# Performance work log

Hardware: AMD Instinct MI355X
Metric: run time of the kernel (lower is better)

Reference implementation:

```python
import jax, jax.numpy as jnp
import numpy as np

IMG, P, C = 224, 16, 3
D, H, MLP = 512, 8, 2048
L, NCLS = 10, 10      # budget, classes
N = (IMG // P) ** 2   # 196 patches
PD = C * P * P        # patch_dim = 768


def setup_inputs() -> dict:
    key = jax.random.key(0)
    ks = jax.random.split(key, 32)
    w = lambda k, shape: (jax.random.normal(k, shape, jnp.float32) * 0.02)
    return {
        'x': jax.random.normal(ks[0], (32, C, IMG, IMG), jnp.float32),
        'y': jax.random.randint(ks[1], (32, 1), 0, NCLS),
        'pos_emb': w(ks[2], (1, N + 1, D)),
        'cls_tok': w(ks[3], (1, 1, D)),
        'Wp': w(ks[4], (D, PD)), 'bp': jnp.zeros((D,), jnp.float32),
        'Wqkv': w(ks[5], (3 * D, D)),
        'Wo': w(ks[6], (D, D)), 'bo': jnp.zeros((D,), jnp.float32),
        'ln1_g': jnp.ones((D,), jnp.float32), 'ln1_b': jnp.zeros((D,), jnp.float32),
        'ln2_g': jnp.ones((D,), jnp.float32), 'ln2_b': jnp.zeros((D,), jnp.float32),
        'W1': w(ks[7], (MLP, D)), 'b1': jnp.zeros((MLP,), jnp.float32),
        'W2': w(ks[8], (D, MLP)), 'b2': jnp.zeros((D,), jnp.float32),
        'lnh_g': jnp.ones((D,), jnp.float32), 'lnh_b': jnp.zeros((D,), jnp.float32),
        'Wh1': w(ks[9], (MLP, D)), 'bh1': jnp.zeros((MLP,), jnp.float32),
        'Wh2': w(ks[10], (1, MLP)), 'bh2': jnp.zeros((1,), jnp.float32),
        'lnc_g': jnp.ones((D,), jnp.float32), 'lnc_b': jnp.zeros((D,), jnp.float32),
        'Wc1': w(ks[11], (MLP, D)), 'bc1': jnp.zeros((MLP,), jnp.float32),
        'Wc2': w(ks[12], (NCLS, MLP)), 'bc2': jnp.zeros((NCLS,), jnp.float32),
    }


def _ln(u, g, b):
    mu = u.mean(-1, keepdims=True)
    v = ((u - mu) ** 2).mean(-1, keepdims=True)
    return (u - mu) / jnp.sqrt(v + 1e-5) * g + b


def _gelu(u):
    return jax.nn.gelu(u, approximate=False)


def reference(x, y, pos_emb, cls_tok, Wp, bp, Wqkv, Wo, bo,
              ln1_g, ln1_b, ln2_g, ln2_b, W1, b1, W2, b2,
              lnh_g, lnh_b, Wh1, bh1, Wh2, bh2,
              lnc_g, lnc_b, Wc1, bc1, Wc2, bc2):
    b = x.shape[0]
    hp = IMG // P
    # patchify: b c (h p1) (w p2) -> b (h w) (p1 p2 c)
    xp = x.reshape(b, C, hp, P, hp, P).transpose(0, 2, 4, 3, 5, 1).reshape(b, N, PD)
    e = xp @ Wp.T + bp                                   # [b, N, D]
    z = jnp.concatenate([jnp.broadcast_to(cls_tok, (b, 1, D)), e], 1) + pos_emb[:, :N + 1]

    scale = D ** -0.5

    def attn(u):
        q, k, v = jnp.split(u @ Wqkv.T, 3, axis=-1)
        hsplit = lambda t: t.reshape(b, -1, H, D // H).transpose(0, 2, 1, 3)  # b h n d
        q, k, v = hsplit(q), hsplit(k), hsplit(v)
        a = jax.nn.softmax(jnp.einsum('bhid,bhjd->bhij', q, k) * scale, axis=-1)
        o = jnp.einsum('bhij,bhjd->bhid', a, v).transpose(0, 2, 1, 3).reshape(b, -1, D)
        return o @ Wo.T + bo

    def ff(u):
        return _gelu(u @ W1.T + b1) @ W2.T + b2

    def halt(u):
        h = _gelu(_ln(u, lnh_g, lnh_b) @ Wh1.T + bh1) @ Wh2.T + bh2  # [b, n, 1]
        return jax.nn.sigmoid(h).mean(1)[:, 0]                        # [b]

    def step(u, _):
        u = u + attn(_ln(u, ln1_g, ln1_b))
        u = u + ff(_ln(u, ln2_g, ln2_b))
        return u, (u[:, 0], halt(u))

    _, (cls_outs, halts) = jax.lax.scan(step, z, None, length=L)
    cls_outs = cls_outs.transpose(1, 0, 2)   # [b, L, D]
    halts = halts.T                          # [b, L]

    logits = _gelu(_ln(cls_outs, lnc_g, lnc_b) @ Wc1.T + bc1) @ Wc2.T + bc2  # [b, L, 10]
    logp = jax.nn.log_softmax(logits, -1)
    lab = y[:, 0]
    ce = -jnp.take_along_axis(logp, jnp.broadcast_to(lab[:, None, None], (b, L, 1)), axis=2)[..., 0]  # [b, L]

    idx = jnp.argmin(ce, axis=1) + 1                     # [b], halting step per sample
    steps = jnp.arange(L)
    mask = (steps[None, :] < idx[:, None]).astype(ce.dtype)
    denom = idx.astype(ce.dtype)
    ref_ce = (ce * mask).sum(1) / denom                  # per-sample mean over first idx steps

    # halt labels: 1 for steps < idx-1, 0 at step idx-1 (only first idx entries count)
    hl = jnp.where(steps[None, :] == (idx[:, None] - 1), 0.0, 1.0)
    p = jnp.clip(halts, 1e-7, 1.0 - 1e-7)
    bce = -(hl * jnp.log(p) + (1.0 - hl) * jnp.log1p(-p))
    halt_loss = (bce * mask).sum(1) / denom

    return ref_ce.mean() + halt_loss.mean()
```

## Files before the change

kernel.cpp:

```cpp
#include <hip/hip_runtime.h>
#include <math.h>

#define BBATCH 32
#define NTOK 197
#define NPATCH 196
#define PDIM 768
#define DDIM 512
#define NHEAD 8
#define DHEAD 64
#define MLPDIM 2048
#define NLAYER 10
#define NCLASS 10
#define MTOK (BBATCH*NTOK)
#define MPAD 6400
#define MPATCH (BBATCH*NPATCH)
#define QKVROWS (MTOK + 16)

typedef unsigned short u16;
typedef __attribute__((ext_vector_type(8))) short bf16x8;
typedef __attribute__((ext_vector_type(4))) float f32x4;
typedef __attribute__((ext_vector_type(8))) unsigned short ushort8;

__device__ __forceinline__ float gelu_f(float x) {
    return 0.5f * x * (1.0f + erff(x * 0.70710678118654752440f));
}
__device__ __forceinline__ float bf2f(u16 u) {
    union { unsigned int i; float f; } v; v.i = ((unsigned int)u) << 16; return v.f;
}
__device__ __forceinline__ u16 f2bf(float f) {
    union { float f; unsigned int u; } v; v.f = f;
    unsigned int r = v.u + 0x7FFFu + ((v.u >> 16) & 1u);
    return (u16)(r >> 16);
}
__device__ __forceinline__ void gload_lds16(const u16* g, u16* l) {
    __builtin_amdgcn_global_load_lds((const __attribute__((address_space(1))) void*)g,
                                     (__attribute__((address_space(3))) void*)l, 16, 0, 0);
}

template<int ACT, int HASB, int HASR, int OUTBF>
__global__ __launch_bounds__(256)
void mgemm_kernel(const u16* __restrict__ A, const u16* __restrict__ W,
                  const float* __restrict__ bias, const float* __restrict__ res,
                  void* __restrict__ Cout, int M, int Nn, int K)
{
    __shared__ u16 As[128 * 64];
    __shared__ u16 Bs[128 * 64];
    const int tid = threadIdx.x;
    const int lane = tid & 63;
    const int wid = tid >> 6;
    const int wr = wid >> 1, wc = wid & 1;
    const int m0 = blockIdx.y * 128, n0 = blockIdx.x * 128;

    f32x4 acc[4][4] = {};

    const int srow = tid >> 3;
    const int dcb  = (tid & 7) << 4;

    for (int k0 = 0; k0 < K; k0 += 64) {
        __syncthreads();
        #pragma unroll
        for (int p = 0; p < 4; ++p) {
            int r = p * 32 + srow;
            int scb = dcb ^ ((r & 7) << 4);
            gload_lds16(A + (size_t)(m0 + r) * K + k0 + (scb >> 1), &As[p * 2048 + tid * 8]);
            gload_lds16(W + (size_t)(n0 + r) * K + k0 + (scb >> 1), &Bs[p * 2048 + tid * 8]);
        }
        __syncthreads();

        #pragma unroll
        for (int kk = 0; kk < 64; kk += 32) {
            const int kb = (kk + ((lane >> 4) << 3)) << 1;
            bf16x8 af[4], bfr[4];
            #pragma unroll
            for (int mi = 0; mi < 4; ++mi) {
                int ar = wr * 64 + mi * 16 + (lane & 15);
                af[mi] = *(const bf16x8*)&As[ar * 64 + ((kb ^ ((ar & 7) << 4)) >> 1)];
            }
            #pragma unroll
            for (int ni = 0; ni < 4; ++ni) {
                int br = wc * 64 + ni * 16 + (lane & 15);
                bfr[ni] = *(const bf16x8*)&Bs[br * 64 + ((kb ^ ((br & 7) << 4)) >> 1)];
            }
            #pragma unroll
            for (int mi = 0; mi < 4; ++mi)
                #pragma unroll
                for (int ni = 0; ni < 4; ++ni)
                    acc[mi][ni] = __builtin_amdgcn_mfma_f32_16x16x32_bf16(
                        af[mi], bfr[ni], acc[mi][ni], 0, 0, 0);
        }
    }

    float* outf = (float*)Cout;
    u16*   outb = (u16*)Cout;
    #pragma unroll
    for (int mi = 0; mi < 4; ++mi) {
        #pragma unroll
        for (int j = 0; j < 4; ++j) {
            int row = m0 + wr * 64 + mi * 16 + ((lane >> 4) << 2) + j;
            if (row >= M) continue;
            #pragma unroll
            for (int ni = 0; ni < 4; ++ni) {
                int col = n0 + wc * 64 + ni * 16 + (lane & 15);
                float v = acc[mi][ni][j];
                if (HASB) v += bias[col];
                if (ACT)  v = gelu_f(v);
                if (HASR) v += res[(size_t)row * Nn + col];
                if (OUTBF) outb[(size_t)row * Nn + col] = f2bf(v);
                else       outf[(size_t)row * Nn + col] = v;
            }
        }
    }
}

__global__ __launch_bounds__(256)
void f2bf_kernel(const float* __restrict__ in, u16* __restrict__ out, int n4)
{
    int i = blockIdx.x * 256 + threadIdx.x;
    if (i >= n4) return;
    float4 v = ((const float4*)in)[i];
    u16 o0 = f2bf(v.x), o1 = f2bf(v.y), o2 = f2bf(v.z), o3 = f2bf(v.w);
    out[i * 4 + 0] = o0; out[i * 4 + 1] = o1; out[i * 4 + 2] = o2; out[i * 4 + 3] = o3;
}

__global__ __launch_bounds__(256)
void ln_kernel(const float* __restrict__ X, const float* __restrict__ g,
               const float* __restrict__ bb, u16* __restrict__ Y, int M)
{
    int wave = (blockIdx.x * 4) + (threadIdx.x >> 6);
    int lane = threadIdx.x & 63;
    if (wave >= M) return;
    const float* x = X + (size_t)wave * DDIM;
    float v[8];
    float s = 0.0f;
    #pragma unroll
    for (int i = 0; i < 8; i++) { v[i] = x[lane + i * 64]; s += v[i]; }
    #pragma unroll
    for (int off = 32; off; off >>= 1) s += __shfl_xor(s, off, 64);
    float mu = s * (1.0f / 512.0f);
    float q = 0.0f;
    #pragma unroll
    for (int i = 0; i < 8; i++) { float d = v[i] - mu; q += d * d; }
    #pragma unroll
    for (int off = 32; off; off >>= 1) q += __shfl_xor(q, off, 64);
    float inv = 1.0f / sqrtf(q * (1.0f / 512.0f) + 1e-5f);
    u16* y = Y + (size_t)wave * DDIM;
    #pragma unroll
    for (int i = 0; i < 8; i++) {
        int c = lane + i * 64;
        y[c] = f2bf((v[i] - mu) * inv * g[c] + bb[c]);
    }
}

__global__ __launch_bounds__(256)
void patch_kernel(const float* __restrict__ x, u16* __restrict__ xp)
{
    size_t idx = (size_t)blockIdx.x * 256 + threadIdx.x;
    if (idx >= (size_t)MPATCH * PDIM) return;
    int pd = (int)(idx % PDIM);
    int bn = (int)(idx / PDIM);
    int n = bn % NPATCH, b = bn / NPATCH;
    int c = pd % 3, pix = pd / 3;
    int px = pix % 16, py = pix / 16;
    int hx = n % 14, hy = n / 14;
    int row = hy * 16 + py, col = hx * 16 + px;
    xp[idx] = f2bf(x[((size_t)(b * 3 + c) * 224 + row) * 224 + col]);
}

__global__ __launch_bounds__(256)
void assemble_kernel(const float* __restrict__ e, const float* __restrict__ clstok,
                     const float* __restrict__ pos, float* __restrict__ U)
{
    size_t idx = (size_t)blockIdx.x * 256 + threadIdx.x;
    if (idx >= (size_t)MTOK * DDIM) return;
    int d = (int)(idx % DDIM);
    int bt = (int)(idx / DDIM);
    int t = bt % NTOK, b = bt / NTOK;
    float v = (t == 0) ? clstok[d] : e[((size_t)b * NPATCH + (t - 1)) * DDIM + d];
    U[idx] = v + pos[t * DDIM + d];
}

__global__ __launch_bounds__(256)
void attn_mfma_kernel(const u16* __restrict__ qkv, u16* __restrict__ O)
{
    __shared__ u16 Ks[208 * 64];
    __shared__ u16 Vt[64 * 208];
    __shared__ u16 Pl[4 * 16 * 208];

    const int bh = blockIdx.x >> 1;
    const int half = blockIdx.x & 1;
    const int b = bh >> 3, h = bh & 7;
    const int tid = threadIdx.x;
    const int lane = tid & 63, wid = tid >> 6;
    const size_t base = ((size_t)b * NTOK) * 1536 + (size_t)h * 64;

    {
        int j0 = tid >> 3;
        int d0 = (tid & 7) * 8;
        for (int p = 0; p < 7; ++p) {
            int j = p * 32 + j0;
            if (j < 208) {
                bf16x8 v = {};
                if (j < NTOK) v = *(const bf16x8*)&qkv[base + (size_t)j * 1536 + 512 + d0];
                int byt = (j * 128 + d0 * 2) ^ ((j & 7) << 4);
                *(bf16x8*)((char*)Ks + byt) = v;
            }
        }
    }
    {
        int d = tid & 63;
        int jg = tid >> 6;
        for (int j = jg * 52; j < jg * 52 + 52; ++j) {
            u16 v = (j < NTOK) ? qkv[base + (size_t)j * 1536 + 1024 + d] : (u16)0;
            int byt = (d * 416 + j * 2) ^ ((d & 7) << 4);
            *(u16*)((char*)Vt + byt) = v;
        }
    }
    __syncthreads();

    u16* Pw = Pl + wid * 16 * 208;
    const float scale = 0.04419417382415922f;
    const int t0   = half ? 7 : 0;
    const int tcnt = half ? 6 : 7;
    const int g = lane >> 4;
    const int mycol = lane & 15;

    for (int ti = wid; ti < tcnt; ti += 4) {
        const int r0 = (t0 + ti) * 16;
        bf16x8 qf[2];
        #pragma unroll
        for (int ks = 0; ks < 2; ++ks) {
            int row = r0 + mycol;
            int col = ks * 32 + (g << 3);
            qf[ks] = *(const bf16x8*)&qkv[base + (size_t)row * 1536 + col];
        }
        f32x4 s[13];
        #pragma unroll
        for (int ct = 0; ct < 13; ++ct) s[ct] = (f32x4){0.f, 0.f, 0.f, 0.f};
        #pragma unroll
        for (int ks = 0; ks < 2; ++ks) {
            int kbyte = (ks * 32 + (g << 3)) * 2;
            #pragma unroll
            for (int ct = 0; ct < 13; ++ct) {
                int n = ct * 16 + mycol;
                bf16x8 kf = *(const bf16x8*)((char*)Ks + ((n * 128 + kbyte) ^ ((n & 7) << 4)));
                s[ct] = __builtin_amdgcn_mfma_f32_16x16x32_bf16(qf[ks], kf, s[ct], 0, 0, 0);
            }
        }
        float m[4], sum[4];
        #pragma unroll
        for (int j = 0; j < 4; ++j) m[j] = -1e30f;
        #pragma unroll
        for (int ct = 0; ct < 13; ++ct) {
            bool valid = (ct * 16 + mycol) < NTOK;
            #pragma unroll
            for (int j = 0; j < 4; ++j) {
                float v = valid ? s[ct][j] * scale : -1e30f;
                s[ct][j] = v;
                m[j] = fmaxf(m[j], v);
            }
        }
        #pragma unroll
        for (int off = 1; off < 16; off <<= 1)
            #pragma unroll
            for (int j = 0; j < 4; ++j) m[j] = fmaxf(m[j], __shfl_xor(m[j], off, 64));
        #pragma unroll
        for (int j = 0; j < 4; ++j) sum[j] = 0.0f;
        #pragma unroll
        for (int ct = 0; ct < 13; ++ct)
            #pragma unroll
            for (int j = 0; j < 4; ++j) {
                float e = expf(s[ct][j] - m[j]);
                s[ct][j] = e;
                sum[j] += e;
            }
        #pragma unroll
        for (int off = 1; off < 16; off <<= 1)
            #pragma unroll
            for (int j = 0; j < 4; ++j) sum[j] += __shfl_xor(sum[j], off, 64);
        float inv[4];
        #pragma unroll
        for (int j = 0; j < 4; ++j) inv[j] = 1.0f / sum[j];
        #pragma unroll
        for (int ct = 0; ct < 13; ++ct) {
            int col = ct * 16 + mycol;
            #pragma unroll
            for (int j = 0; j < 4; ++j) {
                int row = (g << 2) + j;
                int byt = (row * 416 + col * 2) ^ ((row & 7) << 4);
                *(u16*)((char*)Pw + byt) = f2bf(s[ct][j] * inv[j]);
            }
        }
        #pragma unroll
        for (int nt = 0; nt < 4; ++nt) {
            f32x4 o = (f32x4){0.f, 0.f, 0.f, 0.f};
            #pragma unroll
            for (int ks = 0; ks < 7; ++ks) {
                bf16x8 pf = {}, vf = {};
                bool live = !(ks == 6 && g >= 2);
                if (live) {
                    int kbyte = (ks * 32 + (g << 3)) * 2;
                    pf = *(const bf16x8*)((char*)Pw + ((mycol * 416 + kbyte) ^ ((mycol & 7) << 4)));
                    int vrow = nt * 16 + mycol;
                    vf = *(const bf16x8*)((char*)Vt + ((vrow * 416 + kbyte) ^ ((vrow & 7) << 4)));
                }
                o = __builtin_amdgcn_mfma_f32_16x16x32_bf16(pf, vf, o, 0, 0, 0);
            }
            #pragma unroll
            for (int j = 0; j < 4; ++j) {
                int grow = r0 + (g << 2) + j;
                if (grow < NTOK)
                    O[((size_t)b * NTOK + grow) * DDIM + h * 64 + nt * 16 + mycol] = f2bf(o[j]);
            }
        }
    }
}

__global__ __launch_bounds__(256)
void halt_dot_kernel(const u16* __restrict__ Hh, const float* __restrict__ Wh2,
                     const float* __restrict__ bh2, float* __restrict__ hsc)
{
    int wave = (blockIdx.x * 4) + (threadIdx.x >> 6);
    int lane = threadIdx.x & 63;
    if (wave >= MTOK) return;
    const u16* row = Hh + (size_t)wave * MLPDIM;
    float s = 0.0f;
    #pragma unroll
    for (int i = 0; i < 4; i++) {
        ushort8 v = *(const ushort8*)&row[i * 512 + lane * 8];
        #pragma unroll
        for (int j = 0; j < 8; j++)
            s = fmaf(bf2f(v[j]), Wh2[i * 512 + lane * 8 + j], s);
    }
    #pragma unroll
    for (int off = 32; off; off >>= 1) s += __shfl_xor(s, off, 64);
    if (lane == 0) hsc[wave] = 1.0f / (1.0f + expf(-(s + bh2[0])));
}

__global__ __launch_bounds__(64)
void halt_mean_cls_kernel(const float* __restrict__ hsc, const float* __restrict__ U,
                          float* __restrict__ halts, float* __restrict__ cls, int l)
{
    int b = blockIdx.x, lane = threadIdx.x;
    float s = 0.0f;
    for (int t = lane; t < NTOK; t += 64) s += hsc[b * NTOK + t];
    #pragma unroll
    for (int off = 32; off; off >>= 1) s += __shfl_xor(s, off, 64);
    if (lane == 0) halts[b * NLAYER + l] = s * (1.0f / (float)NTOK);
    for (int d = lane; d < DDIM; d += 64)
        cls[((size_t)b * NLAYER + l) * DDIM + d] = U[(size_t)b * NTOK * DDIM + d];
}

__global__ __launch_bounds__(256)
void head_logits_kernel(const u16* __restrict__ Hh, const float* __restrict__ Wc2,
                        const float* __restrict__ bc2, float* __restrict__ logits)
{
    int wave = (blockIdx.x * 4) + (threadIdx.x >> 6);
    int lane = threadIdx.x & 63;
    if (wave >= BBATCH * NLAYER) return;
    const u16* row = Hh + (size_t)wave * MLPDIM;
    float rv[32];
    #pragma unroll
    for (int i = 0; i < 32; i++) rv[i] = bf2f(row[lane + i * 64]);
    #pragma unroll
    for (int c = 0; c < NCLASS; c++) {
        float s = 0.0f;
        #pragma unroll
        for (int i = 0; i < 32; i++) s = fmaf(rv[i], Wc2[c * MLPDIM + lane + i * 64], s);
        #pragma unroll
        for (int off = 32; off; off >>= 1) s += __shfl_xor(s, off, 64);
        if (lane == 0) logits[wave * NCLASS + c] = s + bc2[c];
    }
}

__global__ __launch_bounds__(256)
void ce_kernel(const float* __restrict__ logits, const int* __restrict__ y,
               float* __restrict__ ce)
{
    int r = blockIdx.x * 256 + threadIdx.x;
    if (r >= BBATCH * NLAYER) return;
    const float* lg = logits + (size_t)r * NCLASS;
    float mx = lg[0];
    #pragma unroll
    for (int i = 1; i < NCLASS; i++) mx = fmaxf(mx, lg[i]);
    float s = 0.0f;
    #pragma unroll
    for (int i = 0; i < NCLASS; i++) s += expf(lg[i] - mx);
    int lab = y[r / NLAYER];
    ce[r] = -(lg[lab] - mx - logf(s));
}

__global__ __launch_bounds__(64)
void loss_kernel(const float* __restrict__ ce, const float* __restrict__ halts,
                 float* __restrict__ out)
{
    int b = threadIdx.x;
    float total = 0.0f;
    if (b < BBATCH) {
        const float* c = ce + b * NLAYER;
        int idx = 0; float mn = c[0];
        for (int l = 1; l < NLAYER; l++) if (c[l] < mn) { mn = c[l]; idx = l; }
        idx += 1;
        float acc = 0.0f;
        for (int l = 0; l < idx; l++) {
            acc += c[l];
            float p = halts[b * NLAYER + l];
            p = fminf(fmaxf(p, 1e-7f), 1.0f - 1e-7f);
            float hl = (l == idx - 1) ? 0.0f : 1.0f;
            acc += -(hl * logf(p) + (1.0f - hl) * log1pf(-p));
        }
        total = acc / (float)idx;
    }
    #pragma unroll
    for (int off = 32; off; off >>= 1) total += __shfl_xor(total, off, 64);
    if (threadIdx.x == 0) out[0] = total * (1.0f / (float)BBATCH);
}

extern "C" void kernel_launch(void* const* d_in, const int* in_sizes, int n_in,
                              void* d_out, int out_size, void* d_ws, size_t ws_size,
                              hipStream_t stream)
{
    const float* x      = (const float*)d_in[0];
    const int*   y      = (const int*)d_in[1];
    const float* pos    = (const float*)d_in[2];
    const float* clstok = (const float*)d_in[3];
    const float* Wp     = (const float*)d_in[4];
    const float* bp     = (const float*)d_in[5];
    const float* Wqkv   = (const float*)d_in[6];
    const float* Wo     = (const float*)d_in[7];
    const float* bo     = (const float*)d_in[8];
    const float* ln1g   = (const float*)d_in[9];
    const float* ln1b   = (const float*)d_in[10];
    const float* ln2g   = (const float*)d_in[11];
    const float* ln2b   = (const float*)d_in[12];
    const float* W1     = (const float*)d_in[13];
    const float* b1     = (const float*)d_in[14];
    const float* W2     = (const float*)d_in[15];
    const float* b2     = (const float*)d_in[16];
    const float* lnhg   = (const float*)d_in[17];
    const float* lnhb   = (const float*)d_in[18];
    const float* Wh1    = (const float*)d_in[19];
    const float* bh1    = (const float*)d_in[20];
    const float* Wh2    = (const float*)d_in[21];
    const float* bh2    = (const float*)d_in[22];
    const float* lncg   = (const float*)d_in[23];
    const float* lncb   = (const float*)d_in[24];
    const float* Wc1    = (const float*)d_in[25];
    const float* bc1    = (const float*)d_in[26];
    const float* Wc2    = (const float*)d_in[27];
    const float* bc2    = (const float*)d_in[28];

    float* U      = (float*)d_ws;
    float* EMB    = U + (size_t)MTOK * DDIM;
    float* CLS    = EMB + (size_t)MPATCH * DDIM;
    float* LOGITS = CLS + (size_t)BBATCH * NLAYER * DDIM;
    float* CE     = LOGITS + BBATCH * NLAYER * NCLASS;
    float* HSC    = CE + BBATCH * NLAYER;
    float* HALTS  = HSC + MTOK;
    u16* QKVb = (u16*)(HALTS + BBATCH * NLAYER + 32);
    u16* LNB  = QKVb + (size_t)QKVROWS * 1536;
    u16* HB   = LNB + (size_t)MPAD * DDIM;
    u16* XP   = HB + (size_t)MPAD * MLPDIM;
    u16* CLNB = XP + (size_t)MPATCH * PDIM;
    u16* wWp  = CLNB + 384 * DDIM;
    u16* wWqkv= wWp   + 512 * 768;
    u16* wWo  = wWqkv + 1536 * 512;
    u16* wW1  = wWo   + 512 * 512;
    u16* wW2  = wW1   + 2048 * 512;
    u16* wWh1 = wW2   + 512 * 2048;
    u16* wWc1 = wWh1  + 2048 * 512;

    dim3 blk(256);

    f2bf_kernel<<<dim3((512*768/4 + 255)/256), blk, 0, stream>>>(Wp, wWp, 512*768/4);
    f2bf_kernel<<<dim3((1536*512/4 + 255)/256), blk, 0, stream>>>(Wqkv, wWqkv, 1536*512/4);
    f2bf_kernel<<<dim3((512*512/4 + 255)/256), blk, 0, stream>>>(Wo, wWo, 512*512/4);
    f2bf_kernel<<<dim3((2048*512/4 + 255)/256), blk, 0, stream>>>(W1, wW1, 2048*512/4);
    f2bf_kernel<<<dim3((512*2048/4 + 255)/256), blk, 0, stream>>>(W2, wW2, 512*2048/4);
    f2bf_kernel<<<dim3((2048*512/4 + 255)/256), blk, 0, stream>>>(Wh1, wWh1, 2048*512/4);
    f2bf_kernel<<<dim3((2048*512/4 + 255)/256), blk, 0, stream>>>(Wc1, wWc1, 2048*512/4);

    patch_kernel<<<dim3(((size_t)MPATCH * PDIM + 255) / 256), blk, 0, stream>>>(x, XP);
    mgemm_kernel<0,1,0,0><<<dim3(DDIM/128, MPATCH/128), blk, 0, stream>>>(
        XP, wWp, bp, nullptr, (void*)EMB, MPATCH, DDIM, PDIM);
    assemble_kernel<<<dim3(((size_t)MTOK * DDIM + 255) / 256), blk, 0, stream>>>(
        EMB, clstok, pos, U);

    const int MT = (MTOK + 127) / 128;

    for (int l = 0; l < NLAYER; l++) {
        ln_kernel<<<dim3((MTOK + 3) / 4), blk, 0, stream>>>(U, ln1g, ln1b, LNB, MTOK);
        mgemm_kernel<0,0,0,1><<<dim3(1536/128, MT), blk, 0, stream>>>(
            LNB, wWqkv, nullptr, nullptr, (void*)QKVb, MTOK, 1536, DDIM);
        attn_mfma_kernel<<<dim3(512), blk, 0, stream>>>(QKVb, LNB);
        mgemm_kernel<0,1,1,0><<<dim3(DDIM/128, MT), blk, 0, stream>>>(
            LNB, wWo, bo, U, (void*)U, MTOK, DDIM, DDIM);
        ln_kernel<<<dim3((MTOK + 3) / 4), blk, 0, stream>>>(U, ln2g, ln2b, LNB, MTOK);
        mgemm_kernel<1,1,0,1><<<dim3(MLPDIM/128, MT), blk, 0, stream>>>(
            LNB, wW1, b1, nullptr, (void*)HB, MTOK, MLPDIM, DDIM);
        mgemm_kernel<0,1,1,0><<<dim3(DDIM/128, MT), blk, 0, stream>>>(
            HB, wW2, b2, U, (void*)U, MTOK, DDIM, MLPDIM);
        ln_kernel<<<dim3((MTOK + 3) / 4), blk, 0, stream>>>(U, lnhg, lnhb, LNB, MTOK);
        mgemm_kernel<1,1,0,1><<<dim3(MLPDIM/128, MT), blk, 0, stream>>>(
            LNB, wWh1, bh1, nullptr, (void*)HB, MTOK, MLPDIM, DDIM);
        halt_dot_kernel<<<dim3((MTOK + 3) / 4), blk, 0, stream>>>(HB, Wh2, bh2, HSC);
        halt_mean_cls_kernel<<<dim3(BBATCH), dim3(64), 0, stream>>>(HSC, U, HALTS, CLS, l);
    }

    ln_kernel<<<dim3((BBATCH * NLAYER + 3) / 4), blk, 0, stream>>>(
        CLS, lncg, lncb, CLNB, BBATCH * NLAYER);
    mgemm_kernel<1,1,0,1><<<dim3(MLPDIM/128, 3), blk, 0, stream>>>(
        CLNB, wWc1, bc1, nullptr, (void*)HB, BBATCH * NLAYER, MLPDIM, DDIM);
    head_logits_kernel<<<dim3((BBATCH * NLAYER + 3) / 4), blk, 0, stream>>>(
        HB, Wc2, bc2, LOGITS);
    ce_kernel<<<dim3(2), blk, 0, stream>>>(LOGITS, y, CE);
    loss_kernel<<<dim3(1), dim3(64), 0, stream>>>(CE, HALTS, (float*)d_out);
}
```

Before: 2.419 ms.

## Double-buffer GEMM LDS tiles and fuse halt dot-product into halt GEMM epilogue

The GEMM kernel now uses two LDS buffers, so the next K-tile is loaded while the current one is computed, with a single barrier per iteration. The halting head's second linear layer is folded into the Wh1 GEMM epilogue. Each block computes gelu(acc+bias)·Wh2 partial sums, reduces them across lanes and atomically adds them into a per-token score zeroed by a memset. The sigmoid then moves into the halt-mean kernel. This removes the bf16 HB write and re-read plus a kernel launch, but doubles LDS use (lower occupancy risk) and adds float atomics, which make the summation order non-deterministic.

After: 2.342 ms. 3.2% less time.

```diff
diff --git a/kernel.cpp b/kernel.cpp
--- a/kernel.cpp
+++ b/kernel.cpp
@@ -37,14 +37,14 @@
                                      (__attribute__((address_space(3))) void*)l, 16, 0, 0);
 }
 
-template<int ACT, int HASB, int HASR, int OUTBF>
+template<int ACT, int HASB, int HASR, int OUTBF, int HALT>
 __global__ __launch_bounds__(256)
 void mgemm_kernel(const u16* __restrict__ A, const u16* __restrict__ W,
                   const float* __restrict__ bias, const float* __restrict__ res,
                   void* __restrict__ Cout, int M, int Nn, int K)
 {
-    __shared__ u16 As[128 * 64];
-    __shared__ u16 Bs[128 * 64];
+    __shared__ u16 As[2][128 * 64];
+    __shared__ u16 Bs[2][128 * 64];
     const int tid = threadIdx.x;
     const int lane = tid & 63;
     const int wid = tid >> 6;
@@ -56,17 +56,16 @@
     const int srow = tid >> 3;
     const int dcb  = (tid & 7) << 4;
 
-    for (int k0 = 0; k0 < K; k0 += 64) {
-        __syncthreads();
+    auto stage = [&](int buf, int k0) {
         #pragma unroll
         for (int p = 0; p < 4; ++p) {
             int r = p * 32 + srow;
             int scb = dcb ^ ((r & 7) << 4);
-            gload_lds16(A + (size_t)(m0 + r) * K + k0 + (scb >> 1), &As[p * 2048 + tid * 8]);
-            gload_lds16(W + (size_t)(n0 + r) * K + k0 + (scb >> 1), &Bs[p * 2048 + tid * 8]);
-        }
-        __syncthreads();
-
+            gload_lds16(A + (size_t)(m0 + r) * K + k0 + (scb >> 1), &As[buf][p * 2048 + tid * 8]);
+            gload_lds16(W + (size_t)(n0 + r) * K + k0 + (scb >> 1), &Bs[buf][p * 2048 + tid * 8]);
+        }
+    };
+    auto compute = [&](int buf) {
         #pragma unroll
         for (int kk = 0; kk < 64; kk += 32) {
             const int kb = (kk + ((lane >> 4) << 3)) << 1;
@@ -74,12 +73,12 @@
             #pragma unroll
             for (int mi = 0; mi < 4; ++mi) {
                 int ar = wr * 64 + mi * 16 + (lane & 15);
-                af[mi] = *(const bf16x8*)&As[ar * 64 + ((kb ^ ((ar & 7) << 4)) >> 1)];
+                af[mi] = *(const bf16x8*)&As[buf][ar * 64 + ((kb ^ ((ar & 7) << 4)) >> 1)];
             }
             #pragma unroll
             for (int ni = 0; ni < 4; ++ni) {
                 int br = wc * 64 + ni * 16 + (lane & 15);
-                bfr[ni] = *(const bf16x8*)&Bs[br * 64 + ((kb ^ ((br & 7) << 4)) >> 1)];
+                bfr[ni] = *(const bf16x8*)&Bs[buf][br * 64 + ((kb ^ ((br & 7) << 4)) >> 1)];
             }
             #pragma unroll
             for (int mi = 0; mi < 4; ++mi)
@@ -88,6 +87,44 @@
                     acc[mi][ni] = __builtin_amdgcn_mfma_f32_16x16x32_bf16(
                         af[mi], bfr[ni], acc[mi][ni], 0, 0, 0);
         }
+    };
+
+    const int NT = K >> 6;
+    stage(0, 0);
+    asm volatile("s_waitcnt vmcnt(0)" ::: "memory");
+    __builtin_amdgcn_s_barrier();
+    int cur = 0;
+    #pragma unroll 1
+    for (int t = 0; t < NT - 1; ++t) {
+        stage(cur ^ 1, (t + 1) << 6);
+        compute(cur);
+        asm volatile("s_waitcnt vmcnt(0)" ::: "memory");
+        __builtin_amdgcn_s_barrier();
+        cur ^= 1;
+    }
+    compute(cur);
+
+    if (HALT) {
+        const float* Wh2v = res;
+        float* hout = (float*)Cout;
+        #pragma unroll
+        for (int mi = 0; mi < 4; ++mi) {
+            #pragma unroll
+            for (int j = 0; j < 4; ++j) {
+                int row = m0 + wr * 64 + mi * 16 + ((lane >> 4) << 2) + j;
+                float part = 0.0f;
+                #pragma unroll
+                for (int ni = 0; ni < 4; ++ni) {
+                    int col = n0 + wc * 64 + ni * 16 + (lane & 15);
+                    float v = gelu_f(acc[mi][ni][j] + bias[col]);
+                    part += v * Wh2v[col];
+                }
+                #pragma unroll
+                for (int off = 1; off < 16; off <<= 1) part += __shfl_xor(part, off, 64);
+                if ((lane & 15) == 0 && row < M) atomicAdd(&hout[row], part);
+            }
+        }
+        return;
     }
 
     float* outf = (float*)Cout;
@@ -315,34 +352,18 @@
     }
 }
 
-__global__ __launch_bounds__(256)
-void halt_dot_kernel(const u16* __restrict__ Hh, const float* __restrict__ Wh2,
-                     const float* __restrict__ bh2, float* __restrict__ hsc)
-{
-    int wave = (blockIdx.x * 4) + (threadIdx.x >> 6);
-    int lane = threadIdx.x & 63;
-    if (wave >= MTOK) return;
-    const u16* row = Hh + (size_t)wave * MLPDIM;
+__global__ __launch_bounds__(64)
+void halt_mean_cls_kernel(const float* __restrict__ hsc, const float* __restrict__ bh2,
+                          const float* __restrict__ U,
+                          float* __restrict__ halts, float* __restrict__ cls, int l)
+{
+    int b = blockIdx.x, lane = threadIdx.x;
+    float bb = bh2[0];
     float s = 0.0f;
-    #pragma unroll
-    for (int i = 0; i < 4; i++) {
-        ushort8 v = *(const ushort8*)&row[i * 512 + lane * 8];
-        #pragma unroll
-        for (int j = 0; j < 8; j++)
-            s = fmaf(bf2f(v[j]), Wh2[i * 512 + lane * 8 + j], s);
-    }
-    #pragma unroll
-    for (int off = 32; off; off >>= 1) s += __shfl_xor(s, off, 64);
-    if (lane == 0) hsc[wave] = 1.0f / (1.0f + expf(-(s + bh2[0])));
-}
-
-__global__ __launch_bounds__(64)
-void halt_mean_cls_kernel(const float* __restrict__ hsc, const float* __restrict__ U,
-                          float* __restrict__ halts, float* __restrict__ cls, int l)
-{
-    int b = blockIdx.x, lane = threadIdx.x;
-    float s = 0.0f;
-    for (int t = lane; t < NTOK; t += 64) s += hsc[b * NTOK + t];
+    for (int t = lane; t < NTOK; t += 64) {
+        float raw = hsc[b * NTOK + t] + bb;
+        s += 1.0f / (1.0f + expf(-raw));
+    }
     #pragma unroll
     for (int off = 32; off; off >>= 1) s += __shfl_xor(s, off, 64);
     if (lane == 0) halts[b * NLAYER + l] = s * (1.0f / (float)NTOK);
@@ -480,7 +501,7 @@
     f2bf_kernel<<<dim3((2048*512/4 + 255)/256), blk, 0, stream>>>(Wc1, wWc1, 2048*512/4);
 
     patch_kernel<<<dim3(((size_t)MPATCH * PDIM + 255) / 256), blk, 0, stream>>>(x, XP);
-    mgemm_kernel<0,1,0,0><<<dim3(DDIM/128, MPATCH/128), blk, 0, stream>>>(
+    mgemm_kernel<0,1,0,0,0><<<dim3(DDIM/128, MPATCH/128), blk, 0, stream>>>(
         XP, wWp, bp, nullptr, (void*)EMB, MPATCH, DDIM, PDIM);
     assemble_kernel<<<dim3(((size_t)MTOK * DDIM + 255) / 256), blk, 0, stream>>>(
         EMB, clstok, pos, U);
@@ -489,26 +510,27 @@
 
     for (int l = 0; l < NLAYER; l++) {
         ln_kernel<<<dim3((MTOK + 3) / 4), blk, 0, stream>>>(U, ln1g, ln1b, LNB, MTOK);
-        mgemm_kernel<0,0,0,1><<<dim3(1536/128, MT), blk, 0, stream>>>(
+        mgemm_kernel<0,0,0,1,0><<<dim3(1536/128, MT), blk, 0, stream>>>(
             LNB, wWqkv, nullptr, nullptr, (void*)QKVb, MTOK, 1536, DDIM);
         attn_mfma_kernel<<<dim3(512), blk, 0, stream>>>(QKVb, LNB);
-        mgemm_kernel<0,1,1,0><<<dim3(DDIM/128, MT), blk, 0, stream>>>(
+        mgemm_kernel<0,1,1,0,0><<<dim3(DDIM/128, MT), blk, 0, stream>>>(
             LNB, wWo, bo, U, (void*)U, MTOK, DDIM, DDIM);
         ln_kernel<<<dim3((MTOK + 3) / 4), blk, 0, stream>>>(U, ln2g, ln2b, LNB, MTOK);
-        mgemm_kernel<1,1,0,1><<<dim3(MLPDIM/128, MT), blk, 0, stream>>>(
+        mgemm_kernel<1,1,0,1,0><<<dim3(MLPDIM/128, MT), blk, 0, stream>>>(
             LNB, wW1, b1, nullptr, (void*)HB, MTOK, MLPDIM, DDIM);
-        mgemm_kernel<0,1,1,0><<<dim3(DDIM/128, MT), blk, 0, stream>>>(
+        mgemm_kernel<0,1,1,0,0><<<dim3(DDIM/128, MT), blk, 0, stream>>>(
             HB, wW2, b2, U, (void*)U, MTOK, DDIM, MLPDIM);
         ln_kernel<<<dim3((MTOK + 3) / 4), blk, 0, stream>>>(U, lnhg, lnhb, LNB, MTOK);
-        mgemm_kernel<1,1,0,1><<<dim3(MLPDIM/128, MT), blk, 0, stream>>>(
-            LNB, wWh1, bh1, nullptr, (void*)HB, MTOK, MLPDIM, DDIM);
-        halt_dot_kernel<<<dim3((MTOK + 3) / 4), blk, 0, stream>>>(HB, Wh2, bh2, HSC);
-        halt_mean_cls_kernel<<<dim3(BBATCH), dim3(64), 0, stream>>>(HSC, U, HALTS, CLS, l);
+        hipMemsetAsync(HSC, 0, MTOK * sizeof(float), stream);
+        mgemm_kernel<0,1,0,0,1><<<dim3(MLPDIM/128, MT), blk, 0, stream>>>(
+            LNB, wWh1, bh1, Wh2, (void*)HSC, MTOK, MLPDIM, DDIM);
+        halt_mean_cls_kernel<<<dim3(BBATCH), dim3(64), 0, stream>>>(
+            HSC, bh2, U, HALTS, CLS, l);
     }
 
     ln_kernel<<<dim3((BBATCH * NLAYER + 3) / 4), blk, 0, stream>>>(
         CLS, lncg, lncb, CLNB, BBATCH * NLAYER);
-    mgemm_kernel<1,1,0,1><<<dim3(MLPDIM/128, 3), blk, 0, stream>>>(
+    mgemm_kernel<1,1,0,1,0><<<dim3(MLPDIM/128, 3), blk, 0, stream>>>(
         CLNB, wWc1, bc1, nullptr, (void*)HB, BBATCH * NLAYER, MLPDIM, DDIM);
     head_logits_kernel<<<dim3((BBATCH * NLAYER + 3) / 4), blk, 0, stream>>>(
         HB, Wc2, bc2, LOGITS);
```
